# Performance work log

Measured on AMD Instinct MI355X. Metric: run time of the kernel, lower is better.

## Reference

```python
import jax, jax.numpy as jnp
import numpy as np

B, S, D, H = 2, 4096, 1024, 16
HD = D // H  # 64


def setup_inputs() -> dict:
    key = jax.random.key(0)
    ks = jax.random.split(key, 9)
    init = lambda k, shape: (jax.random.normal(k, shape, dtype=jnp.float32) * 0.02)
    return {
        "x": jax.random.normal(ks[0], (B, S, D), dtype=jnp.float32),
        "Wq": init(ks[1], (D, D)), "bq": init(ks[2], (D,)),
        "Wk": init(ks[3], (D, D)), "bk": init(ks[4], (D,)),
        "Wv": init(ks[5], (D, D)), "bv": init(ks[6], (D,)),
        "Wo": init(ks[7], (D, D)), "bo": init(ks[8], (D,)),
    }


def _split_heads(t):
    # [B, S, D] -> [B, H, S, HD]
    b, s, d = t.shape
    return t.reshape(b, s, H, HD).transpose(0, 2, 1, 3)


def reference(x, Wq, bq, Wk, bk, Wv, bv, Wo, bo):
    # q/k/v projections (torch Linear: x @ W.T + b)
    q = _split_heads(x @ Wq.T + bq)
    k = _split_heads(x @ Wk.T + bk)
    v = _split_heads(x @ Wv.T + bv)
    scale = 1.0 / np.sqrt(HD).astype(np.float32)
    # chunked_attention uses full K/V per chunk => equivalent to full attention.
    scores = jnp.einsum("bhqd,bhkd->bhqk", q, k) * scale
    # softmax computed in fp32 then cast back (matches F.softmax(dtype=float32))
    attn = jax.nn.softmax(scores.astype(jnp.float32), axis=-1).astype(scores.dtype)
    out = jnp.einsum("bhqk,bhkd->bhqd", attn, v)
    out = out.transpose(0, 2, 1, 3).reshape(B, S, D)  # combine heads
    return out @ Wo.T + bo
```

## Files before the change

kernel.cpp:

```cpp
#include <hip/hip_runtime.h>
#include <hip/hip_bf16.h>
#include <stdint.h>

typedef __attribute__((ext_vector_type(8))) short short8;
typedef __attribute__((ext_vector_type(4))) short short4v;
typedef __attribute__((ext_vector_type(4))) float f32x4;

#define MFMA16(A, B, C) __builtin_amdgcn_mfma_f32_16x16x32_bf16(A, B, C, 0, 0, 0)

#define GLDS16(gp, lp) __builtin_amdgcn_global_load_lds(                     \
    (const __attribute__((address_space(1))) unsigned int*)(gp),             \
    (__attribute__((address_space(3))) unsigned int*)(lp), 16, 0, 0)

static constexpr int kS  = 4096;
static constexpr int kD  = 1024;
static constexpr int kH  = 16;
static constexpr int kHD = 64;

__device__ __forceinline__ short bf16_bits(float f) {
    __hip_bfloat16 h = __float2bfloat16(f);
    return *(short*)&h;
}

__device__ __forceinline__ short8 cvt8(const float* __restrict__ p) {
    f32x4 a = ((const f32x4*)p)[0];
    f32x4 b = ((const f32x4*)p)[1];
    short8 r;
    r[0] = bf16_bits(a[0]); r[1] = bf16_bits(a[1]);
    r[2] = bf16_bits(a[2]); r[3] = bf16_bits(a[3]);
    r[4] = bf16_bits(b[0]); r[5] = bf16_bits(b[1]);
    r[6] = bf16_bits(b[2]); r[7] = bf16_bits(b[3]);
    return r;
}

__device__ __forceinline__ unsigned char f32_to_e4m3(float f) {
    unsigned int u = __float_as_uint(f);
    unsigned int s = (u >> 24) & 0x80u;
    unsigned int a = u & 0x7fffffffu;
    if (a < 0x3c800000u) {
        float af = __uint_as_float(a);
        unsigned int sub = (unsigned int)(af * 512.0f + 0.5f);
        return (unsigned char)(s | sub);
    }
    unsigned int r = a + 0x80000u;
    unsigned int m = (r >> 20) & 7u;
    int eb = (int)(r >> 23) - 127 + 7;
    unsigned int bits = ((unsigned int)eb << 3) | m;
    if (bits > 0x7Eu) bits = 0x7Eu;
    return (unsigned char)(s | bits);
}
__device__ __forceinline__ float e4m3_to_f32(unsigned int b) {
    unsigned int s = b & 0x80u;
    unsigned int e = (b >> 3) & 15u;
    unsigned int m = b & 7u;
    float f = e ? __uint_as_float(((e + 120u) << 23) | (m << 20))
                : (float)m * 0.001953125f;
    return s ? -f : f;
}

__global__ __launch_bounds__(256) void cvt_f32_bf16(
    const float* __restrict__ src, __hip_bfloat16* __restrict__ dst)
{
    const int i = blockIdx.x * 256 + threadIdx.x;
    f32x4 v = ((const f32x4*)src)[i];
    short4v o;
    o[0] = bf16_bits(v[0]); o[1] = bf16_bits(v[1]);
    o[2] = bf16_bits(v[2]); o[3] = bf16_bits(v[3]);
    ((short4v*)dst)[i] = o;
}


template <int MODE>
__global__ __launch_bounds__(256) void gemm128(
    const __hip_bfloat16* __restrict__ X, const __hip_bfloat16* __restrict__ W,
    const float* __restrict__ bias, void* __restrict__ outv)
{
    __shared__ short As[128 * 64];
    __shared__ short Bs[128 * 64];

    const int lane = threadIdx.x & 63, wave = threadIdx.x >> 6;
    const int quad = lane >> 4, l16 = lane & 15;
    const int m0 = blockIdx.x * 128, n0 = blockIdx.y * 128;
    const int wm = wave & 1, wn = wave >> 1;

    const short* Xg = (const short*)X + (size_t)m0 * kD;
    const short* Wg = (const short*)W + (size_t)n0 * kD;

    f32x4 acc[4][4];
    #pragma unroll
    for (int mt = 0; mt < 4; ++mt)
        #pragma unroll
        for (int nt = 0; nt < 4; ++nt) acc[mt][nt] = f32x4{0.f, 0.f, 0.f, 0.f};

    const int srow = lane >> 3;
    const int gch  = (lane & 7) ^ srow;

    for (int k0 = 0; k0 < kD; k0 += 64) {
        __syncthreads();
        #pragma unroll
        for (int i = 0; i < 4; ++i) {
            const int rowbase = wave * 32 + i * 8;
            const int row = rowbase + srow;
            GLDS16(Xg + (size_t)row * kD + k0 + gch * 8, &As[rowbase * 64]);
            GLDS16(Wg + (size_t)row * kD + k0 + gch * 8, &Bs[rowbase * 64]);
        }
        __syncthreads();

        #pragma unroll
        for (int c = 0; c < 2; ++c) {
            short8 af[4], bf[4];
            const int rx = l16 & 7;
            #pragma unroll
            for (int mt = 0; mt < 4; ++mt)
                af[mt] = *(const short8*)&As[(wm * 64 + mt * 16 + l16) * 64
                                             + (((c * 4 + quad) ^ rx) * 8)];
            #pragma unroll
            for (int nt = 0; nt < 4; ++nt)
                bf[nt] = *(const short8*)&Bs[(wn * 64 + nt * 16 + l16) * 64
                                             + (((c * 4 + quad) ^ rx) * 8)];
            #pragma unroll
            for (int mt = 0; mt < 4; ++mt)
                #pragma unroll
                for (int nt = 0; nt < 4; ++nt)
                    acc[mt][nt] = MFMA16(af[mt], bf[nt], acc[mt][nt]);
        }
    }

    #pragma unroll
    for (int nt = 0; nt < 4; ++nt) {
        const int n = n0 + wn * 64 + nt * 16 + l16;
        const float bv = bias[n];
        #pragma unroll
        for (int mt = 0; mt < 4; ++mt) {
            #pragma unroll
            for (int r = 0; r < 4; ++r) {
                const int m = m0 + wm * 64 + mt * 16 + quad * 4 + r;
                float v = acc[mt][nt][r] + bv;
                if (MODE == 2) {
                    ((float*)outv)[(size_t)m * kD + n] = v;
                } else {
                    if (MODE == 1) v *= 0.125f;
                    const size_t addr = (((size_t)(m >> 12) * kH + (n >> 6)) * kS
                                         + (size_t)(m & (kS - 1))) * kHD + (size_t)(n & (kHD - 1));
                    ((__hip_bfloat16*)outv)[addr] = __float2bfloat16(v);
                }
            }
        }
    }
}

__global__ __launch_bounds__(256) void transpose_v(
    const __hip_bfloat16* __restrict__ V, __hip_bfloat16* __restrict__ Vt)
{
    __shared__ short T[64][72];
    const int bh = blockIdx.y;
    const int s0 = blockIdx.x * 64;
    const short* src = (const short*)V + ((size_t)bh * kS + s0) * kHD;
    short* dst = (short*)Vt + (size_t)bh * kHD * kS + s0;
    const int tid = threadIdx.x;
    #pragma unroll
    for (int i = 0; i < 2; ++i) {
        const int lin = tid + i * 256, r = lin >> 3, c = lin & 7;
        *(short8*)&T[r][c * 8] = *(const short8*)(src + r * kHD + c * 8);
    }
    __syncthreads();
    #pragma unroll
    for (int i = 0; i < 2; ++i) {
        const int lin = tid + i * 256, d = lin >> 3, sc = lin & 7;
        short8 v;
        #pragma unroll
        for (int j = 0; j < 8; ++j) v[j] = T[sc * 8 + j][d];
        *(short8*)(dst + (size_t)d * kS + sc * 8) = v;
    }
}

__global__ __launch_bounds__(256) void flash2(
    const __hip_bfloat16* __restrict__ Qw, const __hip_bfloat16* __restrict__ Kw,
    const __hip_bfloat16* __restrict__ Vt, __hip_bfloat16* __restrict__ O)
{
    __shared__ short Ks[2][64 * 64];
    __shared__ short Vs[2][64 * 64];
    __shared__ short Ps[4][32][72];
    __shared__ float Ls[4][32];

    const int lane = threadIdx.x & 63, wave = threadIdx.x >> 6;
    const int quad = lane >> 4, l16 = lane & 15;
    const int bh = blockIdx.y, b = bh >> 4, h = bh & 15;
    const int qbase = blockIdx.x * 128 + wave * 32;

    const short* Qg = (const short*)Qw + ((size_t)bh * kS + qbase) * kHD;
    short8 qf[2][2];
    #pragma unroll
    for (int t = 0; t < 2; ++t)
        #pragma unroll
        for (int c = 0; c < 2; ++c)
            qf[t][c] = *(const short8*)(Qg + (t * 16 + l16) * kHD + c * 32 + quad * 8);

    const short* Kg = (const short*)Kw + (size_t)bh * kS * kHD;
    const short* Vg = (const short*)Vt + (size_t)bh * kHD * kS;

    f32x4 o[2][4];
    float lsum[2] = {0.f, 0.f};
    #pragma unroll
    for (int t = 0; t < 2; ++t)
        #pragma unroll
        for (int dt = 0; dt < 4; ++dt) o[t][dt] = f32x4{0.f, 0.f, 0.f, 0.f};

    const int srow = lane >> 3;
    const int gch  = (lane & 7) ^ srow;

    #pragma unroll
    for (int i = 0; i < 2; ++i) {
        const int rowbase = wave * 16 + i * 8;
        const int row = rowbase + srow;
        GLDS16(Kg + (size_t)row * kHD + gch * 8,  &Ks[0][rowbase * 64]);
        GLDS16(Vg + (size_t)row * kS + gch * 8,   &Vs[0][rowbase * 64]);
    }

    for (int k0 = 0; k0 < kS; k0 += 64) {
        const int cur = (k0 >> 6) & 1;
        __syncthreads();
        if (k0 + 64 < kS) {
            const int nxt = cur ^ 1;
            #pragma unroll
            for (int i = 0; i < 2; ++i) {
                const int rowbase = wave * 16 + i * 8;
                const int row = rowbase + srow;
                GLDS16(Kg + (size_t)(k0 + 64 + row) * kHD + gch * 8, &Ks[nxt][rowbase * 64]);
                GLDS16(Vg + (size_t)row * kS + (k0 + 64) + gch * 8,  &Vs[nxt][rowbase * 64]);
            }
        }

        f32x4 sc[2][4];
        const int rx = l16 & 7;
        #pragma unroll
        for (int kt = 0; kt < 4; ++kt) {
            const int row = kt * 16 + l16;
            short8 a0 = *(const short8*)&Ks[cur][row * 64 + ((quad ^ rx) * 8)];
            short8 a1 = *(const short8*)&Ks[cur][row * 64 + (((4 + quad) ^ rx) * 8)];
            f32x4 z = {0.f, 0.f, 0.f, 0.f};
            f32x4 s0 = MFMA16(a0, qf[0][0], z); s0 = MFMA16(a1, qf[0][1], s0);
            f32x4 s1 = MFMA16(a0, qf[1][0], z); s1 = MFMA16(a1, qf[1][1], s1);
            sc[0][kt] = s0; sc[1][kt] = s1;
        }

        #pragma unroll
        for (int t = 0; t < 2; ++t) {
            float lacc = lsum[t];
            #pragma unroll
            for (int kt = 0; kt < 4; ++kt) {
                short4v pk;
                #pragma unroll
                for (int r = 0; r < 4; ++r) {
                    const float s = fminf(sc[t][kt][r], 30.f);
                    const float p = __builtin_amdgcn_exp2f(s * 1.44269504f);
                    lacc += p;
                    pk[r] = bf16_bits(p);
                }
                *(short4v*)&Ps[wave][t * 16 + l16][kt * 16 + quad * 4] = pk;
            }
            lsum[t] = lacc;
        }

        #pragma unroll
        for (int c = 0; c < 2; ++c) {
            short8 pa0 = *(const short8*)&Ps[wave][l16][c * 32 + quad * 8];
            short8 pa1 = *(const short8*)&Ps[wave][16 + l16][c * 32 + quad * 8];
            #pragma unroll
            for (int dt = 0; dt < 4; ++dt) {
                const int d = dt * 16 + l16;
                short8 vb = *(const short8*)&Vs[cur][d * 64 + (((c * 4 + quad) ^ rx) * 8)];
                o[0][dt] = MFMA16(pa0, vb, o[0][dt]);
                o[1][dt] = MFMA16(pa1, vb, o[1][dt]);
            }
        }
    }

    #pragma unroll
    for (int t = 0; t < 2; ++t) {
        float v = lsum[t];
        v += __shfl_xor(v, 16, 64);
        v += __shfl_xor(v, 32, 64);
        Ls[wave][t * 16 + l16] = v;
    }
    #pragma unroll
    for (int t = 0; t < 2; ++t)
        #pragma unroll
        for (int r = 0; r < 4; ++r) {
            const float inv = 1.0f / Ls[wave][t * 16 + quad * 4 + r];
            const int sq = qbase + t * 16 + quad * 4 + r;
            #pragma unroll
            for (int dt = 0; dt < 4; ++dt)
                O[((size_t)b * kS + sq) * kD + h * kHD + dt * 16 + l16] =
                    __float2bfloat16(o[t][dt][r] * inv);
        }
}

template <bool KV8, bool WB16>
__global__ __launch_bounds__(256) void gemm_kv(
    const float* __restrict__ X, const void* __restrict__ W,
    const float* __restrict__ bias, void* __restrict__ outv)
{
    const int lane = threadIdx.x & 63;
    const int wave = threadIdx.x >> 6;
    const int quad = lane >> 4;
    const int l16  = lane & 15;
    const int m0 = blockIdx.x * 16;
    const int n0 = blockIdx.y * 256 + wave * 64;

    const float* xr = X + (size_t)(m0 + l16) * kD;
    const float* wf = (const float*)W + (size_t)(n0 + l16) * kD;
    const short* wb = (const short*)W + (size_t)(n0 + l16) * kD;

    f32x4 acc[4] = {{0.f,0.f,0.f,0.f},{0.f,0.f,0.f,0.f},
                    {0.f,0.f,0.f,0.f},{0.f,0.f,0.f,0.f}};

    for (int k8 = quad; k8 < kD / 8; k8 += 4) {
        short8 a = cvt8(xr + k8 * 8);
        #pragma unroll
        for (int nt = 0; nt < 4; ++nt) {
            short8 w = WB16 ? *(const short8*)(wb + nt * 16 * kD + k8 * 8)
                            : cvt8(wf + nt * 16 * kD + k8 * 8);
            acc[nt] = MFMA16(a, w, acc[nt]);
        }
    }

    #pragma unroll
    for (int nt = 0; nt < 4; ++nt) {
        const int n = n0 + nt * 16 + l16;
        const float bv = bias[n];
        #pragma unroll
        for (int r = 0; r < 4; ++r) {
            const int m = m0 + quad * 4 + r;
            const float v = acc[nt][r] + bv;
            const size_t addr = (((size_t)(m >> 12) * kH + (n >> 6)) * kS
                                 + (size_t)(m & (kS - 1))) * kHD + (size_t)(n & (kHD - 1));
            if (KV8) ((unsigned char*)outv)[addr] = f32_to_e4m3(v);
            else     ((__hip_bfloat16*)outv)[addr] = __float2bfloat16(v);
        }
    }
}

template <bool KV8, bool WB16>
__global__ __launch_bounds__(256) void flash_fusedq(
    const float* __restrict__ x,  const void* __restrict__ Wq,
    const float* __restrict__ bq, const void* __restrict__ Kw,
    const void* __restrict__ Vw,  __hip_bfloat16* __restrict__ O)
{
    __shared__ short pool[9216];
    __shared__ short Ps[4][32][72];

    const int lane = threadIdx.x & 63;
    const int wave = threadIdx.x >> 6;
    const int quad = lane >> 4;
    const int l16  = lane & 15;
    const int bh   = blockIdx.y;
    const int b    = bh >> 4, h = bh & 15;
    const int qbase = blockIdx.x * 128 + wave * 32;

    {
        const float* xr0 = x + (size_t)(b * kS + qbase + l16) * kD;
        const float* xr1 = xr0 + (size_t)16 * kD;
        const float* wqf = (const float*)Wq + (size_t)(h * kHD + l16) * kD;
        const short* wqb = (const short*)Wq + (size_t)(h * kHD + l16) * kD;
        f32x4 qa[2][4];
        #pragma unroll
        for (int t = 0; t < 2; ++t)
            #pragma unroll
            for (int nt = 0; nt < 4; ++nt) qa[t][nt] = f32x4{0.f,0.f,0.f,0.f};

        for (int k8 = quad; k8 < kD / 8; k8 += 4) {
            short8 a0 = cvt8(xr0 + k8 * 8);
            short8 a1 = cvt8(xr1 + k8 * 8);
            #pragma unroll
            for (int nt = 0; nt < 4; ++nt) {
                short8 w = WB16 ? *(const short8*)(wqb + nt * 16 * kD + k8 * 8)
                                : cvt8(wqf + nt * 16 * kD + k8 * 8);
                qa[0][nt] = MFMA16(a0, w, qa[0][nt]);
                qa[1][nt] = MFMA16(a1, w, qa[1][nt]);
            }
        }
        #pragma unroll
        for (int t = 0; t < 2; ++t)
            #pragma unroll
            for (int nt = 0; nt < 4; ++nt) {
                const float bv = bq[h * kHD + nt * 16 + l16];
                #pragma unroll
                for (int r = 0; r < 4; ++r)
                    pool[wave * 2304 + (t * 16 + quad * 4 + r) * 72 + nt * 16 + l16] =
                        bf16_bits((qa[t][nt][r] + bv) * 0.125f);
            }
    }
    short8 qf[2][2];
    #pragma unroll
    for (int t = 0; t < 2; ++t)
        #pragma unroll
        for (int c = 0; c < 2; ++c)
            qf[t][c] = *(const short8*)&pool[wave * 2304 + (t * 16 + l16) * 72 + c * 32 + quad * 8];

    f32x4 o[2][4];
    float mrow[2][4], lrow[2][4];
    #pragma unroll
    for (int t = 0; t < 2; ++t)
        #pragma unroll
        for (int dt = 0; dt < 4; ++dt) o[t][dt] = f32x4{0.f,0.f,0.f,0.f};
    #pragma unroll
    for (int t = 0; t < 2; ++t)
        #pragma unroll
        for (int r = 0; r < 4; ++r) { mrow[t][r] = -INFINITY; lrow[t][r] = 0.f; }

    const __hip_bfloat16* Kb16 = (const __hip_bfloat16*)Kw + (size_t)bh * kS * kHD;
    const __hip_bfloat16* Vb16 = (const __hip_bfloat16*)Vw + (size_t)bh * kS * kHD;
    const unsigned char*  K8   = (const unsigned char*)Kw + (size_t)bh * kS * kHD;
    const unsigned char*  V8   = (const unsigned char*)Vw + (size_t)bh * kS * kHD;

    for (int k0 = 0; k0 < kS; k0 += 64) {
        __syncthreads();
        #pragma unroll
        for (int i = 0; i < 2; ++i) {
            const int lin = threadIdx.x + i * 256;
            const int kr = lin >> 3, c8 = lin & 7;
            short8 kv, vv;
            if (KV8) {
                uint2 kbits = *(const uint2*)(K8 + (size_t)(k0 + kr) * kHD + c8 * 8);
                uint2 vbits = *(const uint2*)(V8 + (size_t)(k0 + kr) * kHD + c8 * 8);
                #pragma unroll
                for (int j = 0; j < 4; ++j) {
                    kv[j]     = bf16_bits(e4m3_to_f32((kbits.x >> (8 * j)) & 255u));
                    kv[4 + j] = bf16_bits(e4m3_to_f32((kbits.y >> (8 * j)) & 255u));
                    vv[j]     = bf16_bits(e4m3_to_f32((vbits.x >> (8 * j)) & 255u));
                    vv[4 + j] = bf16_bits(e4m3_to_f32((vbits.y >> (8 * j)) & 255u));
                }
            } else {
                kv = *(const short8*)(Kb16 + (size_t)(k0 + kr) * kHD + c8 * 8);
                vv = *(const short8*)(Vb16 + (size_t)(k0 + kr) * kHD + c8 * 8);
            }
            *(short8*)&pool[kr * 72 + c8 * 8] = kv;
            #pragma unroll
            for (int j = 0; j < 8; ++j)
                pool[4608 + (c8 * 8 + j) * 72 + (((kr >> 3) ^ c8) << 3) + (kr & 7)] = vv[j];
        }
        __syncthreads();

        f32x4 sc[2][4];
        #pragma unroll
        for (int kt = 0; kt < 4; ++kt) {
            short8 b0 = *(const short8*)&pool[(kt * 16 + l16) * 72 + quad * 8];
            short8 b1 = *(const short8*)&pool[(kt * 16 + l16) * 72 + 32 + quad * 8];
            f32x4 z = {0.f, 0.f, 0.f, 0.f};
            f32x4 s0 = MFMA16(qf[0][0], b0, z); s0 = MFMA16(qf[0][1], b1, s0);
            f32x4 s1 = MFMA16(qf[1][0], b0, z); s1 = MFMA16(qf[1][1], b1, s1);
            sc[0][kt] = s0; sc[1][kt] = s1;
        }

        #pragma unroll
        for (int t = 0; t < 2; ++t)
            #pragma unroll
            for (int r = 0; r < 4; ++r) {
                float s0 = sc[t][0][r], s1 = sc[t][1][r];
                float s2 = sc[t][2][r], s3 = sc[t][3][r];
                float mx = fmaxf(fmaxf(s0, s1), fmaxf(s2, s3));
                #pragma unroll
                for (int off = 1; off < 16; off <<= 1)
                    mx = fmaxf(mx, __shfl_xor(mx, off, 64));
                const float mnew  = fmaxf(mrow[t][r], mx);
                const float alpha = __builtin_amdgcn_exp2f((mrow[t][r] - mnew) * 1.44269504f);
                mrow[t][r] = mnew;
                const float p0 = __builtin_amdgcn_exp2f((s0 - mnew) * 1.44269504f);
                const float p1 = __builtin_amdgcn_exp2f((s1 - mnew) * 1.44269504f);
                const float p2 = __builtin_amdgcn_exp2f((s2 - mnew) * 1.44269504f);
                const float p3 = __builtin_amdgcn_exp2f((s3 - mnew) * 1.44269504f);
                float ps = (p0 + p1) + (p2 + p3);
                #pragma unroll
                for (int off = 1; off < 16; off <<= 1)
                    ps += __shfl_xor(ps, off, 64);
                lrow[t][r] = lrow[t][r] * alpha + ps;
                o[t][0][r] *= alpha; o[t][1][r] *= alpha;
                o[t][2][r] *= alpha; o[t][3][r] *= alpha;
                const int row = t * 16 + quad * 4 + r;
                Ps[wave][row][l16]      = bf16_bits(p0);
                Ps[wave][row][16 + l16] = bf16_bits(p1);
                Ps[wave][row][32 + l16] = bf16_bits(p2);
                Ps[wave][row][48 + l16] = bf16_bits(p3);
            }

        short8 pa[2][2];
        #pragma unroll
        for (int t = 0; t < 2; ++t)
            #pragma unroll
            for (int c = 0; c < 2; ++c)
                pa[t][c] = *(const short8*)&Ps[wave][t * 16 + l16][c * 32 + quad * 8];
        #pragma unroll
        for (int c = 0; c < 2; ++c)
            #pragma unroll
            for (int dt = 0; dt < 4; ++dt) {
                const int d = dt * 16 + l16;
                short8 vb = *(const short8*)&pool[4608 + d * 72 + ((((c * 4 + quad)) ^ (d >> 3)) << 3)];
                o[0][dt] = MFMA16(pa[0][c], vb, o[0][dt]);
                o[1][dt] = MFMA16(pa[1][c], vb, o[1][dt]);
            }
    }

    #pragma unroll
    for (int t = 0; t < 2; ++t)
        #pragma unroll
        for (int r = 0; r < 4; ++r) {
            const float inv = 1.0f / lrow[t][r];
            const int sq = qbase + t * 16 + quad * 4 + r;
            #pragma unroll
            for (int dt = 0; dt < 4; ++dt)
                O[((size_t)b * kS + sq) * kD + h * kHD + dt * 16 + l16] =
                    __float2bfloat16(o[t][dt][r] * inv);
        }
}

template <bool WB16>
__global__ __launch_bounds__(256) void proj_out(
    const __hip_bfloat16* __restrict__ Xb, const void* __restrict__ W,
    const float* __restrict__ bias, float* __restrict__ out)
{
    const int lane = threadIdx.x & 63;
    const int wave = threadIdx.x >> 6;
    const int quad = lane >> 4;
    const int l16  = lane & 15;
    const int m0 = blockIdx.x * 16;
    const int n0 = blockIdx.y * 256 + wave * 64;

    const short8* xr = (const short8*)((const short*)Xb + (size_t)(m0 + l16) * kD);
    const float*  wf = (const float*)W + (size_t)(n0 + l16) * kD;
    const short*  wb = (const short*)W + (size_t)(n0 + l16) * kD;

    f32x4 acc[4] = {{0.f,0.f,0.f,0.f},{0.f,0.f,0.f,0.f},
                    {0.f,0.f,0.f,0.f},{0.f,0.f,0.f,0.f}};

    for (int k8 = quad; k8 < kD / 8; k8 += 4) {
        short8 a = xr[k8];
        #pragma unroll
        for (int nt = 0; nt < 4; ++nt) {
            short8 w = WB16 ? *(const short8*)(wb + nt * 16 * kD + k8 * 8)
                            : cvt8(wf + nt * 16 * kD + k8 * 8);
            acc[nt] = MFMA16(a, w, acc[nt]);
        }
    }

    #pragma unroll
    for (int nt = 0; nt < 4; ++nt) {
        const int n = n0 + nt * 16 + l16;
        const float bv = bias[n];
        #pragma unroll
        for (int r = 0; r < 4; ++r) {
            const int m = m0 + quad * 4 + r;
            out[(size_t)m * kD + n] = acc[nt][r] + bv;
        }
    }
}

extern "C" void kernel_launch(void* const* d_in, const int* in_sizes, int n_in,
                              void* d_out, int out_size, void* d_ws, size_t ws_size,
                              hipStream_t stream)
{
    const float* x = nullptr;
    const float* Wm[4] = {nullptr, nullptr, nullptr, nullptr};
    const float* bm[4] = {nullptr, nullptr, nullptr, nullptr};
    int wi = 0, bi = 0;
    for (int i = 0; i < n_in; ++i) {
        const int s = in_sizes[i];
        if      (s == 2 * kS * kD)         x = (const float*)d_in[i];
        else if (s == kD * kD && wi < 4)   Wm[wi++] = (const float*)d_in[i];
        else if (s == kD      && bi < 4)   bm[bi++] = (const float*)d_in[i];
    }
    const float *Wq = Wm[0], *Wk = Wm[1], *Wv = Wm[2], *Wo = Wm[3];
    const float *bq = bm[0], *bk = bm[1], *bv = bm[2], *bo = bm[3];
    float* out = (float*)d_out;

    const size_t elems = (size_t)2 * kS * kD;
    const size_t wel   = (size_t)kD * kD;
    const size_t MB = 1024 * 1024;
    dim3 bb(256);

    if (ws_size >= 88 * MB) {
        __hip_bfloat16* xb  = (__hip_bfloat16*)d_ws;
        __hip_bfloat16* Qw  = xb + elems;
        __hip_bfloat16* Kw  = Qw + elems;
        __hip_bfloat16* Vw  = Kw + elems;
        __hip_bfloat16* Ow  = Vw + elems;
        __hip_bfloat16* Wqb = Ow + elems;
        __hip_bfloat16* Wkb = Wqb + wel;
        __hip_bfloat16* Wvb = Wkb + wel;
        __hip_bfloat16* Wob = Wvb + wel;

        cvt_f32_bf16<<<dim3(8192), bb, 0, stream>>>(x,  xb);
        cvt_f32_bf16<<<dim3(1024), bb, 0, stream>>>(Wq, Wqb);
        cvt_f32_bf16<<<dim3(1024), bb, 0, stream>>>(Wk, Wkb);
        cvt_f32_bf16<<<dim3(1024), bb, 0, stream>>>(Wv, Wvb);
        cvt_f32_bf16<<<dim3(1024), bb, 0, stream>>>(Wo, Wob);

        dim3 gg(64, 8);
        gemm128<1><<<gg, bb, 0, stream>>>(xb, Wqb, bq, Qw);
        gemm128<0><<<gg, bb, 0, stream>>>(xb, Wkb, bk, Kw);
        gemm128<0><<<gg, bb, 0, stream>>>(xb, Wvb, bv, Vw);
        transpose_v<<<dim3(64, 32), bb, 0, stream>>>(Vw, xb);
        flash2<<<dim3(32, 32), bb, 0, stream>>>(Qw, Kw, xb, Ow);
        gemm128<2><<<gg, bb, 0, stream>>>(Ow, Wob, bo, out);
        return;
    }

    dim3 gg(512, 4), gf(kS / 128, 2 * kH);
    if (ws_size >= 56 * MB) {
        __hip_bfloat16* Kw  = (__hip_bfloat16*)d_ws;
        __hip_bfloat16* Vw  = Kw + elems;
        __hip_bfloat16* Ow  = Vw + elems;
        __hip_bfloat16* Wqb = Ow + elems;
        __hip_bfloat16* Wkb = Wqb + wel;
        __hip_bfloat16* Wvb = Wkb + wel;
        __hip_bfloat16* Wob = Wvb + wel;
        cvt_f32_bf16<<<dim3(1024), bb, 0, stream>>>(Wq, Wqb);
        cvt_f32_bf16<<<dim3(1024), bb, 0, stream>>>(Wk, Wkb);
        cvt_f32_bf16<<<dim3(1024), bb, 0, stream>>>(Wv, Wvb);
        cvt_f32_bf16<<<dim3(1024), bb, 0, stream>>>(Wo, Wob);
        gemm_kv<false, true><<<gg, bb, 0, stream>>>(x, Wkb, bk, Kw);
        gemm_kv<false, true><<<gg, bb, 0, stream>>>(x, Wvb, bv, Vw);
        flash_fusedq<false, true><<<gf, bb, 0, stream>>>(x, Wqb, bq, Kw, Vw, Ow);
        proj_out<true><<<gg, bb, 0, stream>>>(Ow, Wob, bo, out);
    } else if (ws_size >= 48 * MB) {
        __hip_bfloat16* Kw = (__hip_bfloat16*)d_ws;
        __hip_bfloat16* Vw = Kw + elems;
        __hip_bfloat16* Ow = Vw + elems;
        gemm_kv<false, false><<<gg, bb, 0, stream>>>(x, Wk, bk, Kw);
        gemm_kv<false, false><<<gg, bb, 0, stream>>>(x, Wv, bv, Vw);
        flash_fusedq<false, false><<<gf, bb, 0, stream>>>(x, Wq, bq, Kw, Vw, Ow);
        proj_out<false><<<gg, bb, 0, stream>>>(Ow, Wo, bo, out);
    } else {
        unsigned char* Kw = (unsigned char*)d_ws;
        unsigned char* Vw = Kw + elems;
        __hip_bfloat16* Ow = (__hip_bfloat16*)(Vw + elems);
        gemm_kv<true, false><<<gg, bb, 0, stream>>>(x, Wk, bk, Kw);
        gemm_kv<true, false><<<gg, bb, 0, stream>>>(x, Wv, bv, Vw);
        flash_fusedq<true, false><<<gf, bb, 0, stream>>>(x, Wq, bq, Kw, Vw, Ow);
        proj_out<false><<<gg, bb, 0, stream>>>(Ow, Wo, bo, out);
    }
}
```

Measured before the change: 412.1 us.

## Write V transposed from GEMM epilogue, widen flash tile, fold log2e into Q

The V projection GEMM gains a mode that writes V directly in the [bh][d][s] transposed layout with 4-element packed stores, which removes the separate transpose kernel. The attention kernel now processes 64 query rows per wave (256 per block) instead of 32, so each K/V tile loaded into LDS is reused across twice as many MFMAs, and scores are fused straight into exp and P stores. The Q scale now includes log2(e), which removes a multiply before exp2; the clamp is adjusted to match. This costs more registers and LDS per block and halves the grid, which may lower occupancy.

New measurement: 380.6 us. 1.08x faster.

```diff
diff --git a/kernel.cpp b/kernel.cpp
--- a/kernel.cpp
+++ b/kernel.cpp
@@ -132,45 +132,34 @@
         const float bv = bias[n];
         #pragma unroll
         for (int mt = 0; mt < 4; ++mt) {
-            #pragma unroll
-            for (int r = 0; r < 4; ++r) {
-                const int m = m0 + wm * 64 + mt * 16 + quad * 4 + r;
-                float v = acc[mt][nt][r] + bv;
-                if (MODE == 2) {
-                    ((float*)outv)[(size_t)m * kD + n] = v;
-                } else {
-                    if (MODE == 1) v *= 0.125f;
-                    const size_t addr = (((size_t)(m >> 12) * kH + (n >> 6)) * kS
-                                         + (size_t)(m & (kS - 1))) * kHD + (size_t)(n & (kHD - 1));
-                    ((__hip_bfloat16*)outv)[addr] = __float2bfloat16(v);
+            if (MODE == 3) {
+                const int m = m0 + wm * 64 + mt * 16 + quad * 4;
+                short4v pk;
+                #pragma unroll
+                for (int r = 0; r < 4; ++r)
+                    pk[r] = bf16_bits(acc[mt][nt][r] + bv);
+                const int bh2 = (m >> 12) * kH + (n >> 6);
+                short* dst = (short*)outv
+                    + ((size_t)bh2 * kHD + (size_t)(n & (kHD - 1))) * kS
+                    + (size_t)(m & (kS - 1));
+                *(short4v*)dst = pk;
+            } else {
+                #pragma unroll
+                for (int r = 0; r < 4; ++r) {
+                    const int m = m0 + wm * 64 + mt * 16 + quad * 4 + r;
+                    float v = acc[mt][nt][r] + bv;
+                    if (MODE == 2) {
+                        ((float*)outv)[(size_t)m * kD + n] = v;
+                    } else {
+                        if (MODE == 1) v *= 0.18033688f;
+                        const size_t addr = (((size_t)(m >> 12) * kH + (n >> 6)) * kS
+                                             + (size_t)(m & (kS - 1))) * kHD
+                                            + (size_t)(n & (kHD - 1));
+                        ((__hip_bfloat16*)outv)[addr] = __float2bfloat16(v);
+                    }
                 }
             }
         }
-    }
-}
-
-__global__ __launch_bounds__(256) void transpose_v(
-    const __hip_bfloat16* __restrict__ V, __hip_bfloat16* __restrict__ Vt)
-{
-    __shared__ short T[64][72];
-    const int bh = blockIdx.y;
-    const int s0 = blockIdx.x * 64;
-    const short* src = (const short*)V + ((size_t)bh * kS + s0) * kHD;
-    short* dst = (short*)Vt + (size_t)bh * kHD * kS + s0;
-    const int tid = threadIdx.x;
-    #pragma unroll
-    for (int i = 0; i < 2; ++i) {
-        const int lin = tid + i * 256, r = lin >> 3, c = lin & 7;
-        *(short8*)&T[r][c * 8] = *(const short8*)(src + r * kHD + c * 8);
-    }
-    __syncthreads();
-    #pragma unroll
-    for (int i = 0; i < 2; ++i) {
-        const int lin = tid + i * 256, d = lin >> 3, sc = lin & 7;
-        short8 v;
-        #pragma unroll
-        for (int j = 0; j < 8; ++j) v[j] = T[sc * 8 + j][d];
-        *(short8*)(dst + (size_t)d * kS + sc * 8) = v;
     }
 }
 
@@ -180,18 +169,18 @@
 {
     __shared__ short Ks[2][64 * 64];
     __shared__ short Vs[2][64 * 64];
-    __shared__ short Ps[4][32][72];
-    __shared__ float Ls[4][32];
+    __shared__ short Ps[4][64][72];
+    __shared__ float Ls[4][64];
 
     const int lane = threadIdx.x & 63, wave = threadIdx.x >> 6;
     const int quad = lane >> 4, l16 = lane & 15;
     const int bh = blockIdx.y, b = bh >> 4, h = bh & 15;
-    const int qbase = blockIdx.x * 128 + wave * 32;
+    const int qbase = blockIdx.x * 256 + wave * 64;
 
     const short* Qg = (const short*)Qw + ((size_t)bh * kS + qbase) * kHD;
-    short8 qf[2][2];
-    #pragma unroll
-    for (int t = 0; t < 2; ++t)
+    short8 qf[4][2];
+    #pragma unroll
+    for (int t = 0; t < 4; ++t)
         #pragma unroll
         for (int c = 0; c < 2; ++c)
             qf[t][c] = *(const short8*)(Qg + (t * 16 + l16) * kHD + c * 32 + quad * 8);
@@ -199,22 +188,23 @@
     const short* Kg = (const short*)Kw + (size_t)bh * kS * kHD;
     const short* Vg = (const short*)Vt + (size_t)bh * kHD * kS;
 
-    f32x4 o[2][4];
-    float lsum[2] = {0.f, 0.f};
-    #pragma unroll
-    for (int t = 0; t < 2; ++t)
+    f32x4 o[4][4];
+    float lsum[4] = {0.f, 0.f, 0.f, 0.f};
+    #pragma unroll
+    for (int t = 0; t < 4; ++t)
         #pragma unroll
         for (int dt = 0; dt < 4; ++dt) o[t][dt] = f32x4{0.f, 0.f, 0.f, 0.f};
 
     const int srow = lane >> 3;
     const int gch  = (lane & 7) ^ srow;
+    const int rx   = l16 & 7;
 
     #pragma unroll
     for (int i = 0; i < 2; ++i) {
         const int rowbase = wave * 16 + i * 8;
         const int row = rowbase + srow;
-        GLDS16(Kg + (size_t)row * kHD + gch * 8,  &Ks[0][rowbase * 64]);
-        GLDS16(Vg + (size_t)row * kS + gch * 8,   &Vs[0][rowbase * 64]);
+        GLDS16(Kg + (size_t)row * kHD + gch * 8, &Ks[0][rowbase * 64]);
+        GLDS16(Vg + (size_t)row * kS + gch * 8,  &Vs[0][rowbase * 64]);
     }
 
     for (int k0 = 0; k0 < kS; k0 += 64) {
@@ -231,60 +221,55 @@
             }
         }
 
-        f32x4 sc[2][4];
-        const int rx = l16 & 7;
         #pragma unroll
         for (int kt = 0; kt < 4; ++kt) {
             const int row = kt * 16 + l16;
             short8 a0 = *(const short8*)&Ks[cur][row * 64 + ((quad ^ rx) * 8)];
             short8 a1 = *(const short8*)&Ks[cur][row * 64 + (((4 + quad) ^ rx) * 8)];
-            f32x4 z = {0.f, 0.f, 0.f, 0.f};
-            f32x4 s0 = MFMA16(a0, qf[0][0], z); s0 = MFMA16(a1, qf[0][1], s0);
-            f32x4 s1 = MFMA16(a0, qf[1][0], z); s1 = MFMA16(a1, qf[1][1], s1);
-            sc[0][kt] = s0; sc[1][kt] = s1;
-        }
-
-        #pragma unroll
-        for (int t = 0; t < 2; ++t) {
-            float lacc = lsum[t];
-            #pragma unroll
-            for (int kt = 0; kt < 4; ++kt) {
+            #pragma unroll
+            for (int t = 0; t < 4; ++t) {
+                f32x4 z = {0.f, 0.f, 0.f, 0.f};
+                f32x4 s = MFMA16(a0, qf[t][0], z);
+                s = MFMA16(a1, qf[t][1], s);
                 short4v pk;
+                float lacc = 0.f;
                 #pragma unroll
                 for (int r = 0; r < 4; ++r) {
-                    const float s = fminf(sc[t][kt][r], 30.f);
-                    const float p = __builtin_amdgcn_exp2f(s * 1.44269504f);
+                    const float p = __builtin_amdgcn_exp2f(fminf(s[r], 43.f));
                     lacc += p;
                     pk[r] = bf16_bits(p);
                 }
+                lsum[t] += lacc;
                 *(short4v*)&Ps[wave][t * 16 + l16][kt * 16 + quad * 4] = pk;
             }
-            lsum[t] = lacc;
         }
 
         #pragma unroll
         for (int c = 0; c < 2; ++c) {
-            short8 pa0 = *(const short8*)&Ps[wave][l16][c * 32 + quad * 8];
-            short8 pa1 = *(const short8*)&Ps[wave][16 + l16][c * 32 + quad * 8];
+            short8 pa[4];
+            #pragma unroll
+            for (int t = 0; t < 4; ++t)
+                pa[t] = *(const short8*)&Ps[wave][t * 16 + l16][c * 32 + quad * 8];
             #pragma unroll
             for (int dt = 0; dt < 4; ++dt) {
                 const int d = dt * 16 + l16;
                 short8 vb = *(const short8*)&Vs[cur][d * 64 + (((c * 4 + quad) ^ rx) * 8)];
-                o[0][dt] = MFMA16(pa0, vb, o[0][dt]);
-                o[1][dt] = MFMA16(pa1, vb, o[1][dt]);
-            }
-        }
-    }
-
-    #pragma unroll
-    for (int t = 0; t < 2; ++t) {
+                #pragma unroll
+                for (int t = 0; t < 4; ++t)
+                    o[t][dt] = MFMA16(pa[t], vb, o[t][dt]);
+            }
+        }
+    }
+
+    #pragma unroll
+    for (int t = 0; t < 4; ++t) {
         float v = lsum[t];
         v += __shfl_xor(v, 16, 64);
         v += __shfl_xor(v, 32, 64);
         Ls[wave][t * 16 + l16] = v;
     }
     #pragma unroll
-    for (int t = 0; t < 2; ++t)
+    for (int t = 0; t < 4; ++t)
         #pragma unroll
         for (int r = 0; r < 4; ++r) {
             const float inv = 1.0f / Ls[wave][t * 16 + quad * 4 + r];
@@ -582,8 +567,8 @@
         __hip_bfloat16* xb  = (__hip_bfloat16*)d_ws;
         __hip_bfloat16* Qw  = xb + elems;
         __hip_bfloat16* Kw  = Qw + elems;
-        __hip_bfloat16* Vw  = Kw + elems;
-        __hip_bfloat16* Ow  = Vw + elems;
+        __hip_bfloat16* Vtw = Kw + elems;
+        __hip_bfloat16* Ow  = Vtw + elems;
         __hip_bfloat16* Wqb = Ow + elems;
         __hip_bfloat16* Wkb = Wqb + wel;
         __hip_bfloat16* Wvb = Wkb + wel;
@@ -598,9 +583,8 @@
         dim3 gg(64, 8);
         gemm128<1><<<gg, bb, 0, stream>>>(xb, Wqb, bq, Qw);
         gemm128<0><<<gg, bb, 0, stream>>>(xb, Wkb, bk, Kw);
-        gemm128<0><<<gg, bb, 0, stream>>>(xb, Wvb, bv, Vw);
-        transpose_v<<<dim3(64, 32), bb, 0, stream>>>(Vw, xb);
-        flash2<<<dim3(32, 32), bb, 0, stream>>>(Qw, Kw, xb, Ow);
+        gemm128<3><<<gg, bb, 0, stream>>>(xb, Wvb, bv, Vtw);
+        flash2<<<dim3(kS / 256, 32), bb, 0, stream>>>(Qw, Kw, Vtw, Ow);
         gemm128<2><<<gg, bb, 0, stream>>>(Ow, Wob, bo, out);
         return;
     }
```
